# Kernel optimization log

Measured on AMD Instinct MI355X. Metric: run time of the kernel, lower is better.

## Reference

```python
import jax, jax.numpy as jnp
import numpy as np

B, NQ, NKV, D, H, E, FF = 2, 1024, 2048, 1024, 16, 8, 4096
DH = D // H


def _ln(x, g, b):
    m = x.mean(-1, keepdims=True)
    v = ((x - m) ** 2).mean(-1, keepdims=True)
    return (x - m) / jnp.sqrt(v + 1e-5) * g + b


def _mha(q, kv, in_w, in_b, out_w, out_b):
    # torch nn.MultiheadAttention, batch_first=True, dropout=0 (eval)
    wq, wk, wv = jnp.split(in_w, 3, axis=0)   # each [D, D]
    bq, bk, bv = jnp.split(in_b, 3)
    qp = q @ wq.T + bq
    kp = kv @ wk.T + bk
    vp = kv @ wv.T + bv

    def heads(x):
        b, t, _ = x.shape
        return x.reshape(b, t, H, DH).transpose(0, 2, 1, 3)  # [b,H,t,DH]

    qh, kh, vh = heads(qp), heads(kp), heads(vp)
    scores = jnp.einsum('bhqd,bhkd->bhqk', qh, kh) / jnp.sqrt(jnp.float32(DH))
    att = jax.nn.softmax(scores, axis=-1)
    o = jnp.einsum('bhqk,bhkd->bhqd', att, vh)
    o = o.transpose(0, 2, 1, 3).reshape(q.shape[0], q.shape[1], D)
    return o @ out_w.T + out_b


def _moe_token(x, rw, rb, nw, nb, w1, b1, w2, b2, top_k, key):
    # SparseMoE_token: per-token noisy top-k routing.
    logits = x @ rw.T + rb                      # [B,T,E]
    noise_logits = x @ nw.T + nb
    noise = jax.random.normal(key, logits.shape, logits.dtype) * jax.nn.softplus(noise_logits)
    noisy = logits + noise
    _, idx = jax.lax.top_k(noisy, top_k)        # [B,T,K]
    mask = jax.nn.one_hot(idx, E, dtype=noisy.dtype).sum(-2) > 0   # [B,T,E]
    probs = jax.nn.softmax(jnp.where(mask, noisy, -jnp.inf), axis=-1)
    # Dense expert compute weighted by sparse router probs (zeros for
    # non-selected experts) — math identical to masked gather/scatter.
    h = jax.nn.gelu(jnp.einsum('btd,edh->beth', x, w1) + b1[None, :, None, :],
                    approximate=False)          # [B,E,T,FF]
    eo = jnp.einsum('beth,ehd->betd', h, w2) + b2[None, :, None, :]
    return jnp.einsum('bte,betd->btd', probs, eo)


def reference(q, kv,
              ln_cq_g, ln_cq_b, ln_ckv_g, ln_ckv_b, ln_s_g, ln_s_b, ln_m_g, ln_m_b,
              ca_in_w, ca_in_b, ca_out_w, ca_out_b,
              sa_in_w, sa_in_b, sa_out_w, sa_out_b,
              moe_rw, moe_rb, moe_nw, moe_nb, moe_w1, moe_b1, moe_w2, moe_b2,
              top_k):
    key = jax.random.key(42)
    x = _mha(_ln(q, ln_cq_g, ln_cq_b), _ln(kv, ln_ckv_g, ln_ckv_b),
             ca_in_w, ca_in_b, ca_out_w, ca_out_b) + q
    xs = _ln(x, ln_s_g, ln_s_b)
    x = _mha(xs, xs, sa_in_w, sa_in_b, sa_out_w, sa_out_b) + x
    x = _moe_token(_ln(x, ln_m_g, ln_m_b), moe_rw, moe_rb, moe_nw, moe_nb,
                   moe_w1, moe_b1, moe_w2, moe_b2, top_k, key) + x
    return x


def setup_inputs() -> dict:
    key = jax.random.key(0)
    ks = jax.random.split(key, 16)
    s = 0.02
    return {
        'q':  jax.random.normal(ks[0], (B, NQ, D), jnp.float32),
        'kv': jax.random.normal(ks[1], (B, NKV, D), jnp.float32),
        'ln_cq_g': jnp.ones((D,), jnp.float32),  'ln_cq_b': jnp.zeros((D,), jnp.float32),
        'ln_ckv_g': jnp.ones((D,), jnp.float32), 'ln_ckv_b': jnp.zeros((D,), jnp.float32),
        'ln_s_g': jnp.ones((D,), jnp.float32),   'ln_s_b': jnp.zeros((D,), jnp.float32),
        'ln_m_g': jnp.ones((D,), jnp.float32),   'ln_m_b': jnp.zeros((D,), jnp.float32),
        'ca_in_w':  jax.random.normal(ks[2], (3 * D, D), jnp.float32) * s,
        'ca_in_b':  jnp.zeros((3 * D,), jnp.float32),
        'ca_out_w': jax.random.normal(ks[3], (D, D), jnp.float32) * s,
        'ca_out_b': jnp.zeros((D,), jnp.float32),
        'sa_in_w':  jax.random.normal(ks[4], (3 * D, D), jnp.float32) * s,
        'sa_in_b':  jnp.zeros((3 * D,), jnp.float32),
        'sa_out_w': jax.random.normal(ks[5], (D, D), jnp.float32) * s,
        'sa_out_b': jnp.zeros((D,), jnp.float32),
        'moe_rw': jax.random.normal(ks[6], (E, D), jnp.float32) * s,
        'moe_rb': jnp.zeros((E,), jnp.float32),
        'moe_nw': jax.random.normal(ks[7], (E, D), jnp.float32) * s,
        'moe_nb': jnp.zeros((E,), jnp.float32),
        'moe_w1': jax.random.normal(ks[8], (E, D, FF), jnp.float32) * s,
        'moe_b1': jnp.zeros((E, FF), jnp.float32),
        'moe_w2': jax.random.normal(ks[9], (E, FF, D), jnp.float32) * s,
        'moe_b2': jnp.zeros((E, D), jnp.float32),
        'top_k': 2,
    }
```

## Files before the change

### kernel.cpp

```cpp
#include <hip/hip_runtime.h>
#include <cstdint>
#include <cstddef>

#define JAX_THREEFRY_PARTITIONABLE 1

typedef unsigned short u16;
typedef unsigned int u32;
typedef __attribute__((ext_vector_type(8))) short bf16x8;
typedef __attribute__((ext_vector_type(4))) float f32x4;

struct Ptr8 { u16* p[8]; };

struct QkvArgs {
  const u16* ah[3]; const u16* al[3];
  const u16* wh[3]; const u16* wl[3];
  const float* bias[3];
  float* c[3];
  int M[3];
};

__device__ __forceinline__ int imin_(int a, int b) { return a < b ? a : b; }

__device__ __forceinline__ void gl16_(const void* g, void* l) {
  __builtin_amdgcn_global_load_lds(
// ... 67 lines not shown
    p = fmaf(p, w, 0.00134934322f);
    p = fmaf(p, w, -0.00367342844f);
    p = fmaf(p, w, 0.00573950773f);
    p = fmaf(p, w, -0.0076224613f);
    p = fmaf(p, w, 0.00943887047f);
    p = fmaf(p, w, 1.00167406f);
    p = fmaf(p, w, 2.83297682f);
  }
  return p * x;
}

__device__ float bits_to_normal_(unsigned b) {
  const float lo = -0.99999994f;
  float f = __uint_as_float((b >> 9) | 0x3f800000u) - 1.0f;
  float u = fmaxf(lo, f * 2.0f + lo);
  return 1.41421356237f * erfinv_f32_(u);
}

__global__ __launch_bounds__(256) void noise_kernel(float* __restrict__ normals) {
  int i = blockIdx.x * 256 + threadIdx.x;
#if JAX_THREEFRY_PARTITIONABLE
  if (i < 16384) {
    unsigned o0, o1;
    threefry2x32_(0u, 42u, 0u, (unsigned)i, o0, o1);
    normals[i] = bits_to_normal_(o0 ^ o1);
  }
#else
  if (i < 8192) {
    unsigned o0, o1;
    threefry2x32_(0u, 42u, (unsigned)i, (unsigned)(i + 8192), o0, o1);
    normals[i] = bits_to_normal_(o0);
    normals[i + 8192] = bits_to_normal_(o1);
  }
#endif
}

__device__ float block_reduce_sum_(float v) {
  for (int m = 1; m <= 32; m <<= 1) v += __shfl_xor(v, m, 64);
  __shared__ float red[4];
  int lane = threadIdx.x & 63, w = threadIdx.x >> 6;
  if (lane == 0) red[w] = v;
  __syncthreads();
  v = red[0] + red[1] + red[2] + red[3];
  __syncthreads();
  return v;
}

__global__ __launch_bounds__(256) void ln_kernel(
    const float* __restrict__ X, const float* __restrict__ g,
    const float* __restrict__ bta, float* __restrict__ Y) {
  int row = blockIdx.x;
  int t = threadIdx.x;
  const float4* xr = (const float4*)(X + (size_t)row * 1024);
  float4 v = xr[t];
  float s = v.x + v.y + v.z + v.w;
  s = block_reduce_sum_(s);
  float mean = s * (1.0f / 1024.0f);
  float dx = v.x - mean, dy = v.y - mean, dz = v.z - mean, dw = v.w - mean;
  float sq = dx * dx + dy * dy + dz * dz + dw * dw;
  sq = block_reduce_sum_(sq);
  float rstd = 1.0f / sqrtf(sq * (1.0f / 1024.0f) + 1e-5f);
  float4 gv = ((const float4*)g)[t];
  float4 bv = ((const float4*)bta)[t];
  float4 y;
  y.x = dx * rstd * gv.x + bv.x;
  y.y = dy * rstd * gv.y + bv.y;
  y.z = dz * rstd * gv.z + bv.z;
  y.w = dw * rstd * gv.w + bv.w;
  ((float4*)(Y + (size_t)row * 1024))[t] = y;
}

__global__ __launch_bounds__(256) void ln_split_kernel(
    const float* __restrict__ X, const float* __restrict__ g,
    const float* __restrict__ bta, u16* __restrict__ Yh,
    u16* __restrict__ Yl) {
  int row = blockIdx.x;
  int t = threadIdx.x;
  const float4* xr = (const float4*)(X + (size_t)row * 1024);
  float4 v = xr[t];
  float s = v.x + v.y + v.z + v.w;
  s = block_reduce_sum_(s);
  float mean = s * (1.0f / 1024.0f);
  float dx = v.x - mean, dy = v.y - mean, dz = v.z - mean, dw = v.w - mean;
  float sq = dx * dx + dy * dy + dz * dz + dw * dw;
  sq = block_reduce_sum_(sq);
  float rstd = 1.0f / sqrtf(sq * (1.0f / 1024.0f) + 1e-5f);
  float4 gv = ((const float4*)g)[t];
  float4 bv = ((const float4*)bta)[t];
  float y[4];
  y[0] = dx * rstd * gv.x + bv.x;
  y[1] = dy * rstd * gv.y + bv.y;
  y[2] = dz * rstd * gv.z + bv.z;
  y[3] = dw * rstd * gv.w + bv.w;
  ushort4 h, l;
  u16* hp = (u16*)&h; u16* lp = (u16*)&l;
#pragma unroll
  for (int j = 0; j < 4; ++j) {
    u16 hh = f2bf_(y[j]);
    hp[j] = hh;
    lp[j] = f2bf_(y[j] - bf2f_(hh));
  }
  *(ushort4*)(Yh + (size_t)row * 1024 + t * 4) = h;
  *(ushort4*)(Yl + (size_t)row * 1024 + t * 4) = l;
}

__global__ __launch_bounds__(256) void cvt_split_kernel(
    const float* __restrict__ src, u16* __restrict__ hi,
    u16* __restrict__ lo) {
  int i = (blockIdx.x * 256 + threadIdx.x) * 4;
  float4 v = *(const float4*)(src + i);
  float a[4] = {v.x, v.y, v.z, v.w};
  ushort4 h, l;
  u16* hp = (u16*)&h; u16* lp = (u16*)&l;
#pragma unroll
  for (int j = 0; j < 4; ++j) {
    u16 hh = f2bf_(a[j]);
    hp[j] = hh;
    lp[j] = f2bf_(a[j] - bf2f_(hh));
  }
  *(ushort4*)(hi + i) = h;
  *(ushort4*)(lo + i) = l;
}

__global__ __launch_bounds__(256) void tcvt_kernel(
    const float* __restrict__ src, Ptr8 dst, int R, int C) {
  __shared__ float tile[64][65];
  const int e = blockIdx.z;
  const float* S = src + (size_t)e * R * C;
  u16* D = dst.p[e];
  const int c0 = blockIdx.x * 64, r0 = blockIdx.y * 64;
  const int t = threadIdx.x;
  const int tr = t >> 4, tc = (t & 15) * 4;
#pragma unroll
  for (int p = 0; p < 4; ++p) {
    float4 v = *(const float4*)(S + (size_t)(r0 + p * 16 + tr) * C + c0 + tc);
    tile[p * 16 + tr][tc + 0] = v.x;
    tile[p * 16 + tr][tc + 1] = v.y;
    tile[p * 16 + tr][tc + 2] = v.z;
    tile[p * 16 + tr][tc + 3] = v.w;
  }
  __syncthreads();
#pragma unroll
  for (int p = 0; p < 4; ++p) {
    int oc = p * 16 + tr;
    ushort4 o;
    o.x = f2bf_(tile[tc + 0][oc]);
    o.y = f2bf_(tile[tc + 1][oc]);
    o.z = f2bf_(tile[tc + 2][oc]);
    o.w = f2bf_(tile[tc + 3][oc]);
    *(ushort4*)(D + (size_t)(c0 + oc) * R + r0 + tc) = o;
  }
}

template<bool RESID>
__device__ __forceinline__ void split_gemm_body_(
    const u16* __restrict__ Ah, const u16* __restrict__ Al,
    const u16* __restrict__ Wh, const u16* __restrict__ Wl,
    const float* __restrict__ bias, const float* __restrict__ resid,
    float* __restrict__ C, int m0, int n0, int N, int K) {
  __shared__ __align__(16) u16 Ahs[128 * 32];
  __shared__ __align__(16) u16 Als[128 * 32];
  __shared__ __align__(16) u16 Bhs[128 * 32];
  __shared__ __align__(16) u16 Bls[128 * 32];
  const int t = threadIdx.x;
  const int lane = t & 63, wv = t >> 6;
  const int wm = (wv & 1) * 64, wn = (wv >> 1) * 64;
  const int col = lane & 15, quad = lane >> 4;
  f32x4 acc[4][4] = {};
  const int r0 = t >> 2, kq = (t & 3) * 8;
  const u16* pah0 = Ah + (size_t)(m0 + r0) * K + kq;
  const u16* pah1 = Ah + (size_t)(m0 + r0 + 64) * K + kq;
  const u16* pal0 = Al + (size_t)(m0 + r0) * K + kq;
  const u16* pal1 = Al + (size_t)(m0 + r0 + 64) * K + kq;
  const u16* pwh0 = Wh + (size_t)(n0 + r0) * K + kq;
  const u16* pwh1 = Wh + (size_t)(n0 + r0 + 64) * K + kq;
  const u16* pwl0 = Wl + (size_t)(n0 + r0) * K + kq;
  const u16* pwl1 = Wl + (size_t)(n0 + r0 + 64) * K + kq;
  u16* lah0 = &Ahs[t * 8];       u16* lah1 = &Ahs[(t + 256) * 8];
  u16* lal0 = &Als[t * 8];       u16* lal1 = &Als[(t + 256) * 8];
  u16* lbh0 = &Bhs[t * 8];       u16* lbh1 = &Bhs[(t + 256) * 8];
  u16* lbl0 = &Bls[t * 8];       u16* lbl1 = &Bls[(t + 256) * 8];
  for (int k0 = 0; k0 < K; k0 += 32) {
    gl16_(pah0, lah0); gl16_(pah1, lah1);
    gl16_(pal0, lal0); gl16_(pal1, lal1);
    gl16_(pwh0, lbh0); gl16_(pwh1, lbh1);
    gl16_(pwl0, lbl0); gl16_(pwl1, lbl1);
    pah0 += 32; pah1 += 32; pal0 += 32; pal1 += 32;
    pwh0 += 32; pwh1 += 32; pwl0 += 32; pwl1 += 32;
    __syncthreads();
    bf16x8 afh[4], afl[4], bfh[4], bfl[4];
#pragma unroll
    for (int i = 0; i < 4; ++i) {
      afh[i] = *(const bf16x8*)&Ahs[(wm + i * 16 + col) * 32 + quad * 8];
      afl[i] = *(const bf16x8*)&Als[(wm + i * 16 + col) * 32 + quad * 8];
    }
#pragma unroll
    for (int j = 0; j < 4; ++j) {
      bfh[j] = *(const bf16x8*)&Bhs[(wn + j * 16 + col) * 32 + quad * 8];
      bfl[j] = *(const bf16x8*)&Bls[(wn + j * 16 + col) * 32 + quad * 8];
    }
#pragma unroll
    for (int i = 0; i < 4; ++i) {
#pragma unroll
      for (int j = 0; j < 4; ++j) {
        acc[i][j] = __builtin_amdgcn_mfma_f32_16x16x32_bf16(afh[i], bfh[j], acc[i][j], 0, 0, 0);
        acc[i][j] = __builtin_amdgcn_mfma_f32_16x16x32_bf16(afh[i], bfl[j], acc[i][j], 0, 0, 0);
        acc[i][j] = __builtin_amdgcn_mfma_f32_16x16x32_bf16(afl[i], bfh[j], acc[i][j], 0, 0, 0);
      }
    }
    __syncthreads();
  }
  float bv[4];
#pragma unroll
  for (int j = 0; j < 4; ++j) bv[j] = bias[n0 + wn + j * 16 + col];
#pragma unroll
  for (int i = 0; i < 4; ++i) {
#pragma unroll
    for (int rr = 0; rr < 4; ++rr) {
      int m = m0 + wm + i * 16 + quad * 4 + rr;
      float* crow = C + (size_t)m * N;
      const float* rrow = RESID ? (resid + (size_t)m * N) : nullptr;
#pragma unroll
      for (int j = 0; j < 4; ++j) {
        int n = n0 + wn + j * 16 + col;
        float v = acc[i][j][rr] + bv[j];
        if (RESID) v += rrow[n];
        crow[n] = v;
      }
    }
  }
}

template<bool RESID>
__global__ __launch_bounds__(256) void split_gemm_nt(
    const u16* __restrict__ Ah, const u16* __restrict__ Al,
    const u16* __restrict__ Wh, const u16* __restrict__ Wl,
    const float* __restrict__ bias, const float* __restrict__ resid,
    float* __restrict__ C, int M, int N, int K) {
  (void)M;
  split_gemm_body_<RESID>(Ah, Al, Wh, Wl, bias, resid, C,
                          blockIdx.y * 128, blockIdx.x * 128, N, K);
}

__global__ __launch_bounds__(256) void split_gemm_qkv(QkvArgs a, int N, int K) {
  const int z = blockIdx.z;
  const int m0 = blockIdx.y * 128;
  if (m0 >= a.M[z]) return;
  split_gemm_body_<false>(a.ah[z], a.al[z], a.wh[z], a.wl[z], a.bias[z],
                          nullptr, a.c[z], m0, blockIdx.x * 128, N, K);
}

__global__ __launch_bounds__(256) void attn_kernel(
    const float* __restrict__ QP, const float* __restrict__ KP,
    const float* __restrict__ VP, u16* __restrict__ AOh,
    u16* __restrict__ AOl, int nq, int nkv) {
  __shared__ __align__(16) u16 Ksh[64 * 72];
  __shared__ __align__(16) u16 Ksl[64 * 72];
  __shared__ __align__(16) u16 Vth[64 * 72];
  __shared__ __align__(16) u16 Vtl[64 * 72];
  const int t = threadIdx.x;
  const int lane = t & 63, wv = t >> 6;
  const int col = lane & 15, quad = lane >> 4;
  const int bh = blockIdx.x;
  const int b = bh >> 4, h = bh & 15;
  const int q0 = blockIdx.y * 64;
  const int wq0 = wv * 16;

  bf16x8 qbh[2], qbl[2];
  {
    const float* qsrc =
        QP + (size_t)(b * nq + q0 + wq0 + col) * 1024 + h * 64 + quad * 8;
#pragma unroll
    for (int ks = 0; ks < 2; ++ks) {
      float4 f0 = *(const float4*)(qsrc + ks * 32);
      float4 f1 = *(const float4*)(qsrc + ks * 32 + 4);
      float qf[8] = {f0.x, f0.y, f0.z, f0.w, f1.x, f1.y, f1.z, f1.w};
      FragU uh, ul;
#pragma unroll
      for (int w = 0; w < 4; ++w)
        split2_(qf[2 * w] * 0.125f, qf[2 * w + 1] * 0.125f, uh.w[w], ul.w[w]);
      qbh[ks] = uh.v;
      qbl[ks] = ul.v;
    }
  }

  f32x4 o[4] = {};
  float mi = -INFINITY, li = 0.0f;

  const int kr = t >> 2, kc = (t & 3) * 16;
  const int vg = t >> 5, vr = (t & 31) * 2;

  for (int kv0 = 0; kv0 < nkv; kv0 += 64) {
    {
      const float* ksrc =
          KP + (size_t)(b * nkv + kv0 + kr) * 1024 + h * 64 + kc;
      float4 f0 = *(const float4*)(ksrc);
      float4 f1 = *(const float4*)(ksrc + 4);
      float4 f2 = *(const float4*)(ksrc + 8);
      float4 f3 = *(const float4*)(ksrc + 12);
      float kf[16] = {f0.x, f0.y, f0.z, f0.w, f1.x, f1.y, f1.z, f1.w,
                      f2.x, f2.y, f2.z, f2.w, f3.x, f3.y, f3.z, f3.w};
      FragU h0, h1, l0, l1;
#pragma unroll
      for (int w = 0; w < 4; ++w) {
        split2_(kf[2 * w], kf[2 * w + 1], h0.w[w], l0.w[w]);
        split2_(kf[8 + 2 * w], kf[9 + 2 * w], h1.w[w], l1.w[w]);
      }
      *(uint4*)&Ksh[kr * 72 + kc] = h0.q;
      *(uint4*)&Ksh[kr * 72 + kc + 8] = h1.q;
      *(uint4*)&Ksl[kr * 72 + kc] = l0.q;
      *(uint4*)&Ksl[kr * 72 + kc + 8] = l1.q;
    }
    {
      const float* vsrc =
          VP + (size_t)(b * nkv + kv0 + vr) * 1024 + h * 64 + vg * 8;
      float4 a0 = *(const float4*)(vsrc);
      float4 a1 = *(const float4*)(vsrc + 4);
      float4 b0 = *(const float4*)(vsrc + 1024);
      float4 b1 = *(const float4*)(vsrc + 1028);
      float va[8] = {a0.x, a0.y, a0.z, a0.w, a1.x, a1.y, a1.z, a1.w};
      float vb[8] = {b0.x, b0.y, b0.z, b0.w, b1.x, b1.y, b1.z, b1.w};
#pragma unroll
      for (int e = 0; e < 8; ++e) {
        u32 hh, ll;
        split2_(va[e], vb[e], hh, ll);
        *(u32*)&Vth[(vg * 8 + e) * 72 + vr] = hh;
        *(u32*)&Vtl[(vg * 8 + e) * 72 + vr] = ll;
      }
    }
    __syncthreads();

    f32x4 st[4] = {};
#pragma unroll
    for (int ks = 0; ks < 2; ++ks) {
      bf16x8 kah[4], kal[4];
#pragma unroll
      for (int i = 0; i < 4; ++i) {
        kah[i] = *(const bf16x8*)&Ksh[(i * 16 + col) * 72 + ks * 32 + quad * 8];
        kal[i] = *(const bf16x8*)&Ksl[(i * 16 + col) * 72 + ks * 32 + quad * 8];
      }
#pragma unroll
      for (int i = 0; i < 4; ++i) {
        st[i] = __builtin_amdgcn_mfma_f32_16x16x32_bf16(kah[i], qbh[ks], st[i], 0, 0, 0);
        st[i] = __builtin_amdgcn_mfma_f32_16x16x32_bf16(kah[i], qbl[ks], st[i], 0, 0, 0);
        st[i] = __builtin_amdgcn_mfma_f32_16x16x32_bf16(kal[i], qbh[ks], st[i], 0, 0, 0);
      }
    }

    float tmax = st[0][0];
#pragma unroll
    for (int i = 0; i < 4; ++i)
#pragma unroll
      for (int r = 0; r < 4; ++r) tmax = fmaxf(tmax, st[i][r]);
    tmax = fmaxf(tmax, __shfl_xor(tmax, 16, 64));
    tmax = fmaxf(tmax, __shfl_xor(tmax, 32, 64));
    float mnew = fmaxf(mi, tmax);
    float alpha = __expf(mi - mnew);
    float tsum = 0.0f;
#pragma unroll
    for (int i = 0; i < 4; ++i) {
#pragma unroll
      for (int r = 0; r < 4; ++r) {
        float p = __expf(st[i][r] - mnew);
        st[i][r] = p;
        tsum += p;
      }
    }
    tsum += __shfl_xor(tsum, 16, 64);
    tsum += __shfl_xor(tsum, 32, 64);
    li = li * alpha + tsum;
    mi = mnew;
    float alr[4];
#pragma unroll
    for (int r = 0; r < 4; ++r)
      alr[r] = __shfl(alpha, (lane & 48) | (quad * 4 + r), 64);
#pragma unroll
    for (int j = 0; j < 4; ++j)
#pragma unroll
      for (int r = 0; r < 4; ++r) o[j][r] *= alr[r];

    u32 pkh[4][2], pkl[4][2];
#pragma unroll
    for (int i = 0; i < 4; ++i)
#pragma unroll
      for (int w = 0; w < 2; ++w)
        split2_(st[i][2 * w], st[i][2 * w + 1], pkh[i][w], pkl[i][w]);
    u32 APh[2][4], APl[2][4];
    const int par = quad >> 1;
#pragma unroll
    for (int i = 0; i < 4; ++i) {
#pragma unroll
      for (int w01 = 0; w01 < 2; ++w01) {
#pragma unroll
        for (int dw = 0; dw < 2; ++dw) {
          int src = (((2 * quad + dw) & 3) << 4) | col;
          u32 vh = (u32)__shfl((int)pkh[i][w01], src, 64);
          u32 vl = (u32)__shfl((int)pkl[i][w01], src, 64);
          if ((i & 1) == par) {
            APh[i >> 1][dw * 2 + w01] = vh;
            APl[i >> 1][dw * 2 + w01] = vl;
          }
        }
      }
    }

#pragma unroll
    for (int ks = 0; ks < 2; ++ks) {
      FragU fh, fl;
#pragma unroll
      for (int w = 0; w < 4; ++w) { fh.w[w] = APh[ks][w]; fl.w[w] = APl[ks][w]; }
      bf16x8 pah = fh.v, pal = fl.v;
#pragma unroll
      for (int j = 0; j < 4; ++j) {
        bf16x8 vbh = *(const bf16x8*)&Vth[(j * 16 + col) * 72 + ks * 32 + quad * 8];
        bf16x8 vbl = *(const bf16x8*)&Vtl[(j * 16 + col) * 72 + ks * 32 + quad * 8];
        o[j] = __builtin_amdgcn_mfma_f32_16x16x32_bf16(pah, vbh, o[j], 0, 0, 0);
        o[j] = __builtin_amdgcn_mfma_f32_16x16x32_bf16(pah, vbl, o[j], 0, 0, 0);
        o[j] = __builtin_amdgcn_mfma_f32_16x16x32_bf16(pal, vbh, o[j], 0, 0, 0);
      }
    }
    __syncthreads();
  }

  float inv = 1.0f / li;
  float ivr[4];
#pragma unroll
  for (int r = 0; r < 4; ++r)
    ivr[r] = __shfl(inv, (lane & 48) | (quad * 4 + r), 64);
#pragma unroll
  for (int r = 0; r < 4; ++r) {
    size_t base =
        (size_t)(b * nq + q0 + wq0 + quad * 4 + r) * 1024 + h * 64 + col;
#pragma unroll
    for (int j = 0; j < 4; ++j) {
      float v = o[j][r] * ivr[r];
      u16 hh = f2bf_(v);
      AOh[base + j * 16] = hh;
      AOl[base + j * 16] = f2bf_(v - bf2f_(hh));
    }
  }
}

__global__ __launch_bounds__(256) void router_kernel(
    const float* __restrict__ xm, const float* __restrict__ rw,
    const float* __restrict__ rb, const float* __restrict__ nw,
    const float* __restrict__ nb, float* __restrict__ logits,
    float* __restrict__ nlogits) {
  int row = blockIdx.x, t = threadIdx.x;
  const float* x = xm + (size_t)row * 1024;
  float accl[8] = {}, accn[8] = {};
  for (int d = t; d < 1024; d += 256) {
    float xv = x[d];
#pragma unroll
    for (int e = 0; e < 8; ++e) {
      accl[e] += xv * rw[e * 1024 + d];
      accn[e] += xv * nw[e * 1024 + d];
    }
  }
  __shared__ float red[16][4];
  int lane = t & 63, w = t >> 6;
#pragma unroll
  for (int e = 0; e < 8; ++e) {
    float v = accl[e];
    for (int m = 1; m <= 32; m <<= 1) v += __shfl_xor(v, m, 64);
    if (lane == 0) red[e][w] = v;
    float v2 = accn[e];
    for (int m = 1; m <= 32; m <<= 1) v2 += __shfl_xor(v2, m, 64);
    if (lane == 0) red[8 + e][w] = v2;
  }
  __syncthreads();
  if (t < 8)
    logits[row * 8 + t] = red[t][0] + red[t][1] + red[t][2] + red[t][3] + rb[t];
  else if (t < 16)
    nlogits[row * 8 + t - 8] =
        red[t][0] + red[t][1] + red[t][2] + red[t][3] + nb[t - 8];
}

__global__ __launch_bounds__(256) void route_kernel(
    const float* __restrict__ logits, const float* __restrict__ nlogits,
    const float* __restrict__ normals, int* __restrict__ routei,
    float* __restrict__ routep, int* __restrict__ cnt) {
  int bt = blockIdx.x * 256 + threadIdx.x;
  if (bt >= 2048) return;
  float noisy[8];
#pragma unroll
  for (int e = 0; e < 8; ++e) {
    float nl = nlogits[bt * 8 + e];
    float sp = fmaxf(nl, 0.0f) + log1pf(expf(-fabsf(nl)));
    noisy[e] = logits[bt * 8 + e] + normals[bt * 8 + e] * sp;
  }
  int i1 = 0; float n1 = noisy[0];
#pragma unroll
  for (int e = 1; e < 8; ++e) if (noisy[e] > n1) { n1 = noisy[e]; i1 = e; }
  int i2 = -1; float n2 = -INFINITY;
#pragma unroll
  for (int e = 0; e < 8; ++e)
    if (e != i1 && noisy[e] > n2) { n2 = noisy[e]; i2 = e; }
  float e2 = expf(n2 - n1);
  float denom = 1.0f + e2;
  routei[bt * 2 + 0] = i1; routei[bt * 2 + 1] = i2;
  routep[bt * 2 + 0] = 1.0f / denom; routep[bt * 2 + 1] = e2 / denom;
  atomicAdd(&cnt[i1], 1);
  atomicAdd(&cnt[i2], 1);
}

__global__ void zero_kernel(int* __restrict__ cnt) {
  if (threadIdx.x < 8) cnt[threadIdx.x] = 0;
}

__global__ void offs_kernel(const int* __restrict__ cnt, int* __restrict__ offs,
                            int* __restrict__ fill) {
  if (threadIdx.x == 0 && blockIdx.x == 0) {
    int o = 0;
    for (int e = 0; e < 8; ++e) { offs[e] = o; o += cnt[e]; fill[e] = 0; }
  }
}

__global__ __launch_bounds__(256) void fill_kernel(
    const int* __restrict__ routei, const float* __restrict__ routep,
    const int* __restrict__ offs, int* __restrict__ fill,
    int* __restrict__ alist, float* __restrict__ aprob) {
  int bt = blockIdx.x * 256 + threadIdx.x;
  if (bt >= 2048) return;
#pragma unroll
  for (int s = 0; s < 2; ++s) {
    int e = routei[bt * 2 + s];
    int pos = offs[e] + atomicAdd(&fill[e], 1);
    alist[pos] = bt;
    aprob[pos] = routep[bt * 2 + s];
  }
}

__global__ __launch_bounds__(256) void copy_kernel(const float* __restrict__ src,
                                                   float* __restrict__ dst) {
  int i = blockIdx.x * 256 + threadIdx.x;
  ((float4*)dst)[i] = ((const float4*)src)[i];
}

__global__ __launch_bounds__(256) void f2bf_kernel(const float* __restrict__ src,
                                                   u16* __restrict__ dst) {
  int i = (blockIdx.x * 256 + threadIdx.x) * 4;
  float4 v = *(const float4*)(src + i);
  ushort4 o;
  o.x = f2bf_(v.x); o.y = f2bf_(v.y); o.z = f2bf_(v.z); o.w = f2bf_(v.w);
  *(ushort4*)(dst + i) = o;
}

__device__ __forceinline__ float gelu_exact_(float x) {
  return 0.5f * x * (1.0f + erff(x * 0.70710678f));
}

__global__ __launch_bounds__(256) void ffn1_mfma(
    const u16* __restrict__ Xb, Ptr8 w1t, const float* __restrict__ B1,
    u16* __restrict__ H, const int* __restrict__ alist,
    const int* __restrict__ cnt, const int* __restrict__ offs) {
  const int e = blockIdx.z;
  const int ce = cnt[e];
  const int m0 = blockIdx.y * 128;
  if (m0 >= ce) return;
  const int off = offs[e];
  const int n0 = blockIdx.x * 128;
  const u16* __restrict__ WT = w1t.p[e];
  __shared__ __align__(16) u16 As[128 * 32];
  __shared__ __align__(16) u16 Bs[128 * 32];
  const int t = threadIdx.x;
  const int lane = t & 63, wv = t >> 6;
  const int wm = (wv & 1) * 64, wn = (wv >> 1) * 64;
  const int col = lane & 15, quad = lane >> 4;
  f32x4 acc[4][4] = {};
  const int r0 = t >> 2, kq = (t & 3) * 8;
  const int arow0 = alist[off + imin_(m0 + r0, ce - 1)];
  const int arow1 = alist[off + imin_(m0 + r0 + 64, ce - 1)];
  const u16* pa0 = Xb + (size_t)arow0 * 1024 + kq;
  const u16* pa1 = Xb + (size_t)arow1 * 1024 + kq;
  const u16* pw0 = WT + (size_t)(n0 + r0) * 1024 + kq;
  const u16* pw1 = WT + (size_t)(n0 + r0 + 64) * 1024 + kq;
  u16* la0 = &As[t * 8]; u16* la1 = &As[(t + 256) * 8];
  u16* lb0 = &Bs[t * 8]; u16* lb1 = &Bs[(t + 256) * 8];
  for (int k0 = 0; k0 < 1024; k0 += 32) {
    gl16_(pa0, la0); gl16_(pa1, la1);
    gl16_(pw0, lb0); gl16_(pw1, lb1);
    pa0 += 32; pa1 += 32; pw0 += 32; pw1 += 32;
    __syncthreads();
    bf16x8 af[4], bf[4];
#pragma unroll
    for (int i = 0; i < 4; ++i)
      af[i] = *(const bf16x8*)&As[(wm + i * 16 + col) * 32 + quad * 8];
#pragma unroll
    for (int j = 0; j < 4; ++j)
      bf[j] = *(const bf16x8*)&Bs[(wn + j * 16 + col) * 32 + quad * 8];
#pragma unroll
    for (int i = 0; i < 4; ++i)
#pragma unroll
      for (int j = 0; j < 4; ++j)
        acc[i][j] = __builtin_amdgcn_mfma_f32_16x16x32_bf16(af[i], bf[j], acc[i][j], 0, 0, 0);
    __syncthreads();
  }
#pragma unroll
  for (int j = 0; j < 4; ++j) {
    int n = n0 + wn + j * 16 + col;
    float bv = B1[(size_t)e * 4096 + n];
#pragma unroll
    for (int i = 0; i < 4; ++i) {
#pragma unroll
      for (int r2 = 0; r2 < 4; ++r2) {
        int m = m0 + wm + i * 16 + quad * 4 + r2;
        if (m < ce) {
          float v = gelu_exact_(acc[i][j][r2] + bv);
          H[(size_t)(off + m) * 4096 + n] = f2bf_(v);
        }
      }
    }
  }
}

__global__ __launch_bounds__(256) void ffn2_mfma(
    const u16* __restrict__ H, Ptr8 w2t, const float* __restrict__ B2,
    float* __restrict__ Out, const int* __restrict__ alist,
    const float* __restrict__ aprob, const int* __restrict__ cnt,
    const int* __restrict__ offs) {
  const int e = blockIdx.z;
  const int ce = cnt[e];
  const int mt = blockIdx.y >> 2, ks = blockIdx.y & 3;
  const int m0 = mt * 128;
  if (m0 >= ce) return;
  const int off = offs[e];
  const int n0 = blockIdx.x * 128;
  const u16* __restrict__ WT = w2t.p[e];
  __shared__ __align__(16) u16 As[128 * 32];
  __shared__ __align__(16) u16 Bs[128 * 32];
  const int t = threadIdx.x;
  const int lane = t & 63, wv = t >> 6;
  const int wm = (wv & 1) * 64, wn = (wv >> 1) * 64;
  const int col = lane & 15, quad = lane >> 4;
  f32x4 acc[4][4] = {};
  const int r0 = t >> 2, kq = (t & 3) * 8;
  const u16* pa0 =
      H + (size_t)(off + imin_(m0 + r0, ce - 1)) * 4096 + ks * 1024 + kq;
  const u16* pa1 =
      H + (size_t)(off + imin_(m0 + r0 + 64, ce - 1)) * 4096 + ks * 1024 + kq;
  const u16* pw0 = WT + (size_t)(n0 + r0) * 4096 + ks * 1024 + kq;
  const u16* pw1 = WT + (size_t)(n0 + r0 + 64) * 4096 + ks * 1024 + kq;
  u16* la0 = &As[t * 8]; u16* la1 = &As[(t + 256) * 8];
  u16* lb0 = &Bs[t * 8]; u16* lb1 = &Bs[(t + 256) * 8];
  for (int k0 = 0; k0 < 1024; k0 += 32) {
    gl16_(pa0, la0); gl16_(pa1, la1);
    gl16_(pw0, lb0); gl16_(pw1, lb1);
    pa0 += 32; pa1 += 32; pw0 += 32; pw1 += 32;
    __syncthreads();
    bf16x8 af[4], bf[4];
#pragma unroll
    for (int i = 0; i < 4; ++i)
      af[i] = *(const bf16x8*)&As[(wm + i * 16 + col) * 32 + quad * 8];
#pragma unroll
    for (int j = 0; j < 4; ++j)
      bf[j] = *(const bf16x8*)&Bs[(wn + j * 16 + col) * 32 + quad * 8];
#pragma unroll
    for (int i = 0; i < 4; ++i)
#pragma unroll
      for (int j = 0; j < 4; ++j)
        acc[i][j] = __builtin_amdgcn_mfma_f32_16x16x32_bf16(af[i], bf[j], acc[i][j], 0, 0, 0);
    __syncthreads();
  }
  float bv[4];
#pragma unroll
  for (int j = 0; j < 4; ++j)
    bv[j] = (ks == 0) ? B2[(size_t)e * 1024 + n0 + wn + j * 16 + col] : 0.0f;
#pragma unroll
  for (int i = 0; i < 4; ++i) {
#pragma unroll
    for (int r2 = 0; r2 < 4; ++r2) {
      int m = m0 + wm + i * 16 + quad * 4 + r2;
      if (m < ce) {
        int aidx = off + m;
        int tok = alist[aidx];
        float p = aprob[aidx];
        float* orow = Out + (size_t)tok * 1024;
#pragma unroll
        for (int j = 0; j < 4; ++j) {
          int n = n0 + wn + j * 16 + col;
          atomicAdd(&orow[n], p * (acc[i][j][r2] + bv[j]));
        }
      }
    }
  }
}

extern "C" void kernel_launch(void* const* d_in, const int* in_sizes, int n_in,
                              void* d_out, int out_size, void* d_ws, size_t ws_size,
                              hipStream_t stream) {
  (void)in_sizes; (void)n_in; (void)out_size; (void)ws_size;
  const float* q        = (const float*)d_in[0];
  const float* kv       = (const float*)d_in[1];
  const float* ln_cq_g  = (const float*)d_in[2];
  const float* ln_cq_b  = (const float*)d_in[3];
  const float* ln_ckv_g = (const float*)d_in[4];
  const float* ln_ckv_b = (const float*)d_in[5];
  const float* ln_s_g   = (const float*)d_in[6];
  const float* ln_s_b   = (const float*)d_in[7];
  const float* ln_m_g   = (const float*)d_in[8];
  const float* ln_m_b   = (const float*)d_in[9];
  const float* ca_in_w  = (const float*)d_in[10];
  const float* ca_in_b  = (const float*)d_in[11];
  const float* ca_out_w = (const float*)d_in[12];
  const float* ca_out_b = (const float*)d_in[13];
  const float* sa_in_w  = (const float*)d_in[14];
  const float* sa_in_b  = (const float*)d_in[15];
  const float* sa_out_w = (const float*)d_in[16];
  const float* sa_out_b = (const float*)d_in[17];
  const float* moe_rw   = (const float*)d_in[18];
  const float* moe_rb   = (const float*)d_in[19];
  const float* moe_nw   = (const float*)d_in[20];
  const float* moe_nb   = (const float*)d_in[21];
  const float* moe_w1   = (const float*)d_in[22];
  const float* moe_b1   = (const float*)d_in[23];
  const float* moe_w2   = (const float*)d_in[24];
  const float* moe_b2   = (const float*)d_in[25];
  float* out = (float*)d_out;

  float* ws = (float*)d_ws;
  const size_t MEG = 1u << 20;
  float* x1   = ws;
  float* x2   = ws + 2 * MEG;
  float* xm   = ws + 4 * MEG;
  u16*   aoh  = (u16*)(ws + 6 * MEG);
  u16*   aol  = (u16*)(ws + 7 * MEG);
  float* misc = ws + 8 * MEG;
  float* normals = misc;
  float* logits  = misc + 16384;
  float* nlogits = misc + 32768;
  float* routep  = misc + 49152;
  float* aprob   = misc + 53248;
  int*   routei  = (int*)(misc + 57344);
  int*   alist   = (int*)(misc + 61440);
  int*   cnt     = (int*)(misc + 65536);
  int*   offs    = cnt + 8;
  int*   fillc   = cnt + 16;
  float* RA = ws + 8 * MEG + 131072;
  u16*   w1h = (u16*)RA;
  u16*   w1l = (u16*)(RA + (3 * MEG) / 2);
  u16*   w2h = (u16*)(RA + 3 * MEG);
  u16*   w2l = (u16*)(RA + 3 * MEG + MEG / 2);
  u16*   a1h = (u16*)(RA + 4 * MEG);
  u16*   a1l = (u16*)(RA + 5 * MEG);
  u16*   a2h = (u16*)(RA + 6 * MEG);
  u16*   a2l = (u16*)(RA + 8 * MEG);
  float* qp  = RA + 10 * MEG;
  float* kp  = RA + 12 * MEG;
  float* vp  = RA + 16 * MEG;
  u16*   xb  = (u16*)RA;
  u16*   hb  = (u16*)(RA + 1 * MEG);
  Ptr8 wt;
  wt.p[0] = (u16*)(RA + 9 * MEG);
  wt.p[1] = (u16*)(RA + 11 * MEG);
  wt.p[2] = (u16*)(RA + 13 * MEG);
  wt.p[3] = (u16*)(RA + 15 * MEG);
  wt.p[4] = (u16*)(RA + 17 * MEG);
  wt.p[5] = (u16*)x1;
  wt.p[6] = (u16*)xm;
  wt.p[7] = (u16*)(ws + 6 * MEG);

  dim3 blk(256);

  zero_kernel<<<dim3(1), blk, 0, stream>>>(cnt);
  noise_kernel<<<dim3(64), blk, 0, stream>>>(normals);

  cvt_split_kernel<<<dim3(3072), blk, 0, stream>>>(ca_in_w, w1h, w1l);
  cvt_split_kernel<<<dim3(1024), blk, 0, stream>>>(ca_out_w, w2h, w2l);
  ln_split_kernel<<<dim3(2048), blk, 0, stream>>>(q, ln_cq_g, ln_cq_b, a1h, a1l);
  ln_split_kernel<<<dim3(4096), blk, 0, stream>>>(kv, ln_ckv_g, ln_ckv_b, a2h, a2l);
  {
    QkvArgs qa;
    qa.ah[0] = a1h; qa.al[0] = a1l;
    qa.ah[1] = a2h; qa.al[1] = a2l;
    qa.ah[2] = a2h; qa.al[2] = a2l;
    for (int z = 0; z < 3; ++z) {
      qa.wh[z] = w1h + (size_t)z * MEG;
      qa.wl[z] = w1l + (size_t)z * MEG;
      qa.bias[z] = ca_in_b + z * 1024;
    }
    qa.c[0] = qp; qa.c[1] = kp; qa.c[2] = vp;
    qa.M[0] = 2048; qa.M[1] = 4096; qa.M[2] = 4096;
    split_gemm_qkv<<<dim3(8, 32, 3), blk, 0, stream>>>(qa, 1024, 1024);
  }
  attn_kernel<<<dim3(32, 16), blk, 0, stream>>>(qp, kp, vp, aoh, aol, 1024, 2048);
  split_gemm_nt<true><<<dim3(8, 16), blk, 0, stream>>>(
      aoh, aol, w2h, w2l, ca_out_b, q, x1, 2048, 1024, 1024);

  cvt_split_kernel<<<dim3(3072), blk, 0, stream>>>(sa_in_w, w1h, w1l);
  cvt_split_kernel<<<dim3(1024), blk, 0, stream>>>(sa_out_w, w2h, w2l);
  ln_split_kernel<<<dim3(2048), blk, 0, stream>>>(x1, ln_s_g, ln_s_b, a1h, a1l);
  {
    QkvArgs qa;
    for (int z = 0; z < 3; ++z) {
      qa.ah[z] = a1h; qa.al[z] = a1l;
      qa.wh[z] = w1h + (size_t)z * MEG;
      qa.wl[z] = w1l + (size_t)z * MEG;
      qa.bias[z] = sa_in_b + z * 1024;
      qa.M[z] = 2048;
    }
    qa.c[0] = qp; qa.c[1] = kp; qa.c[2] = vp;
    split_gemm_qkv<<<dim3(8, 16, 3), blk, 0, stream>>>(qa, 1024, 1024);
  }
  attn_kernel<<<dim3(32, 16), blk, 0, stream>>>(qp, kp, vp, aoh, aol, 1024, 1024);
  split_gemm_nt<true><<<dim3(8, 16), blk, 0, stream>>>(
      aoh, aol, w2h, w2l, sa_out_b, x1, x2, 2048, 1024, 1024);

  ln_kernel<<<dim3(2048), blk, 0, stream>>>(x2, ln_m_g, ln_m_b, xm);
  f2bf_kernel<<<dim3(2048), blk, 0, stream>>>(xm, xb);
  router_kernel<<<dim3(2048), blk, 0, stream>>>(xm, moe_rw, moe_rb, moe_nw, moe_nb, logits, nlogits);
  route_kernel<<<dim3(8), blk, 0, stream>>>(logits, nlogits, normals, routei, routep, cnt);
  offs_kernel<<<dim3(1), blk, 0, stream>>>(cnt, offs, fillc);
  fill_kernel<<<dim3(8), blk, 0, stream>>>(routei, routep, offs, fillc, alist, aprob);
  copy_kernel<<<dim3(2048), blk, 0, stream>>>(x2, out);
  tcvt_kernel<<<dim3(64, 16, 8), blk, 0, stream>>>(moe_w1, wt, 1024, 4096);
  ffn1_mfma<<<dim3(32, 16, 8), blk, 0, stream>>>(xb, wt, moe_b1, hb, alist, cnt, offs);
  tcvt_kernel<<<dim3(16, 64, 8), blk, 0, stream>>>(moe_w2, wt, 4096, 1024);
  ffn2_mfma<<<dim3(8, 64, 8), blk, 0, stream>>>(hb, wt, moe_b2, out, alist, aprob, cnt, offs);
}
```

Before: 1.069 ms.

## Pre-split K/V into swizzled bf16, prefetch tiles, split-K atomic out-proj

```diff
diff --git a/kernel.cpp b/kernel.cpp
--- a/kernel.cpp
+++ b/kernel.cpp
@@ -243,12 +243,79 @@
   }
 }
 
-template<bool RESID>
+__global__ __launch_bounds__(256) void ksp_k_kernel(
+    const float* __restrict__ KP, u16* __restrict__ Kh,
+    u16* __restrict__ Kl, int nkv) {
+  const int bh = blockIdx.x;
+  const int b = bh >> 4, h = bh & 15;
+  const int kv0 = blockIdx.y * 64;
+  const int t = threadIdx.x;
+  const int kvl = t >> 2, dh0 = (t & 3) * 16;
+  const int kv = kv0 + kvl;
+  const float* src = KP + (size_t)(b * nkv + kv) * 1024 + h * 64 + dh0;
+  float f[16];
+  *(float4*)(f + 0)  = *(const float4*)(src + 0);
+  *(float4*)(f + 4)  = *(const float4*)(src + 4);
+  *(float4*)(f + 8)  = *(const float4*)(src + 8);
+  *(float4*)(f + 12) = *(const float4*)(src + 12);
+  size_t rowb = ((size_t)bh * nkv + kv) * 64;
+#pragma unroll
+  for (int pi = 0; pi < 2; ++pi) {
+    int p = (t & 3) * 2 + pi;
+    FragU hq, lq;
+#pragma unroll
+    for (int w = 0; w < 4; ++w)
+      split2_(f[pi * 8 + 2 * w], f[pi * 8 + 2 * w + 1], hq.w[w], lq.w[w]);
+    int q = p ^ (kvl & 7);
+    *(uint4*)&Kh[rowb + q * 8] = hq.q;
+    *(uint4*)&Kl[rowb + q * 8] = lq.q;
+  }
+}
+
+__global__ __launch_bounds__(256) void ksp_v_kernel(
+    const float* __restrict__ VP, u16* __restrict__ Vh,
+    u16* __restrict__ Vl, int nkv) {
+  __shared__ float tile[64][65];
+  const int bh = blockIdx.x;
+  const int b = bh >> 4, h = bh & 15;
+  const int kv0 = blockIdx.y * 64;
+  const int t = threadIdx.x;
+  {
+    const int kvl = t >> 2, dh0 = (t & 3) * 16;
+    const float* src =
+        VP + (size_t)(b * nkv + kv0 + kvl) * 1024 + h * 64 + dh0;
+#pragma unroll
+    for (int j = 0; j < 4; ++j) {
+      float4 v = *(const float4*)(src + 4 * j);
+      tile[kvl][dh0 + 4 * j + 0] = v.x;
+      tile[kvl][dh0 + 4 * j + 1] = v.y;
+      tile[kvl][dh0 + 4 * j + 2] = v.z;
+      tile[kvl][dh0 + 4 * j + 3] = v.w;
+    }
+  }
+  __syncthreads();
+  const int dh = t >> 2;
+  size_t rowb = ((size_t)bh * 64 + dh) * nkv + kv0;
+#pragma unroll
+  for (int pi = 0; pi < 2; ++pi) {
+    int p = (t & 3) * 2 + pi;
+    FragU hq, lq;
+#pragma unroll
+    for (int w = 0; w < 4; ++w)
+      split2_(tile[p * 8 + 2 * w][dh], tile[p * 8 + 2 * w + 1][dh],
+              hq.w[w], lq.w[w]);
+    int q = p ^ (dh & 7);
+    *(uint4*)&Vh[rowb + q * 8] = hq.q;
+    *(uint4*)&Vl[rowb + q * 8] = lq.q;
+  }
+}
+
+template<bool ATOMIC>
 __device__ __forceinline__ void split_gemm_body_(
     const u16* __restrict__ Ah, const u16* __restrict__ Al,
     const u16* __restrict__ Wh, const u16* __restrict__ Wl,
-    const float* __restrict__ bias, const float* __restrict__ resid,
-    float* __restrict__ C, int m0, int n0, int N, int K) {
+    const float* __restrict__ bias, int addb, float* __restrict__ C,
+    int m0, int n0, int N, int K, int kbeg, int klen) {
   __shared__ __align__(16) u16 Ahs[128 * 32];
   __shared__ __align__(16) u16 Als[128 * 32];
   __shared__ __align__(16) u16 Bhs[128 * 32];
@@ -259,25 +326,27 @@
   const int col = lane & 15, quad = lane >> 4;
   f32x4 acc[4][4] = {};
   const int r0 = t >> 2, kq = (t & 3) * 8;
-  const u16* pah0 = Ah + (size_t)(m0 + r0) * K + kq;
-  const u16* pah1 = Ah + (size_t)(m0 + r0 + 64) * K + kq;
-  const u16* pal0 = Al + (size_t)(m0 + r0) * K + kq;
-  const u16* pal1 = Al + (size_t)(m0 + r0 + 64) * K + kq;
-  const u16* pwh0 = Wh + (size_t)(n0 + r0) * K + kq;
-  const u16* pwh1 = Wh + (size_t)(n0 + r0 + 64) * K + kq;
-  const u16* pwl0 = Wl + (size_t)(n0 + r0) * K + kq;
-  const u16* pwl1 = Wl + (size_t)(n0 + r0 + 64) * K + kq;
-  u16* lah0 = &Ahs[t * 8];       u16* lah1 = &Ahs[(t + 256) * 8];
-  u16* lal0 = &Als[t * 8];       u16* lal1 = &Als[(t + 256) * 8];
-  u16* lbh0 = &Bhs[t * 8];       u16* lbh1 = &Bhs[(t + 256) * 8];
-  u16* lbl0 = &Bls[t * 8];       u16* lbl1 = &Bls[(t + 256) * 8];
-  for (int k0 = 0; k0 < K; k0 += 32) {
-    gl16_(pah0, lah0); gl16_(pah1, lah1);
-    gl16_(pal0, lal0); gl16_(pal1, lal1);
-    gl16_(pwh0, lbh0); gl16_(pwh1, lbh1);
-    gl16_(pwl0, lbl0); gl16_(pwl1, lbl1);
-    pah0 += 32; pah1 += 32; pal0 += 32; pal1 += 32;
-    pwh0 += 32; pwh1 += 32; pwl0 += 32; pwl1 += 32;
+  const u16* pah0 = Ah + (size_t)(m0 + r0) * K + kbeg + kq;
+  const u16* pah1 = Ah + (size_t)(m0 + r0 + 64) * K + kbeg + kq;
+  const u16* pal0 = Al + (size_t)(m0 + r0) * K + kbeg + kq;
+  const u16* pal1 = Al + (size_t)(m0 + r0 + 64) * K + kbeg + kq;
+  const u16* pwh0 = Wh + (size_t)(n0 + r0) * K + kbeg + kq;
+  const u16* pwh1 = Wh + (size_t)(n0 + r0 + 64) * K + kbeg + kq;
+  const u16* pwl0 = Wl + (size_t)(n0 + r0) * K + kbeg + kq;
+  const u16* pwl1 = Wl + (size_t)(n0 + r0 + 64) * K + kbeg + kq;
+  u16* lah0 = &Ahs[t * 8]; u16* lah1 = &Ahs[(t + 256) * 8];
+  u16* lal0 = &Als[t * 8]; u16* lal1 = &Als[(t + 256) * 8];
+  u16* lbh0 = &Bhs[t * 8]; u16* lbh1 = &Bhs[(t + 256) * 8];
+  u16* lbl0 = &Bls[t * 8]; u16* lbl1 = &Bls[(t + 256) * 8];
+#define SG_ISSUE() do { \
+    gl16_(pah0, lah0); gl16_(pah1, lah1); \
+    gl16_(pal0, lal0); gl16_(pal1, lal1); \
+    gl16_(pwh0, lbh0); gl16_(pwh1, lbh1); \
+    gl16_(pwl0, lbl0); gl16_(pwl1, lbl1); \
+    pah0 += 32; pah1 += 32; pal0 += 32; pal1 += 32; \
+    pwh0 += 32; pwh1 += 32; pwl0 += 32; pwl1 += 32; } while (0)
+  SG_ISSUE();
+  for (int k0 = 0; k0 < klen; k0 += 32) {
     __syncthreads();
     bf16x8 afh[4], afl[4], bfh[4], bfl[4];
 #pragma unroll
@@ -290,6 +359,8 @@
       bfh[j] = *(const bf16x8*)&Bhs[(wn + j * 16 + col) * 32 + quad * 8];
       bfl[j] = *(const bf16x8*)&Bls[(wn + j * 16 + col) * 32 + quad * 8];
     }
+    __syncthreads();
+    if (k0 + 32 < klen) SG_ISSUE();
 #pragma unroll
     for (int i = 0; i < 4; ++i) {
 #pragma unroll
@@ -299,56 +370,56 @@
         acc[i][j] = __builtin_amdgcn_mfma_f32_16x16x32_bf16(afl[i], bfh[j], acc[i][j], 0, 0, 0);
       }
     }
-    __syncthreads();
-  }
+  }
+#undef SG_ISSUE
   float bv[4];
 #pragma unroll
-  for (int j = 0; j < 4; ++j) bv[j] = bias[n0 + wn + j * 16 + col];
+  for (int j = 0; j < 4; ++j)
+    bv[j] = (!ATOMIC || addb) ? bias[n0 + wn + j * 16 + col] : 0.0f;
 #pragma unroll
   for (int i = 0; i < 4; ++i) {
 #pragma unroll
     for (int rr = 0; rr < 4; ++rr) {
       int m = m0 + wm + i * 16 + quad * 4 + rr;
       float* crow = C + (size_t)m * N;
-      const float* rrow = RESID ? (resid + (size_t)m * N) : nullptr;
 #pragma unroll
       for (int j = 0; j < 4; ++j) {
         int n = n0 + wn + j * 16 + col;
         float v = acc[i][j][rr] + bv[j];
-        if (RESID) v += rrow[n];
-        crow[n] = v;
+        if (ATOMIC) atomicAdd(&crow[n], v);
+        else crow[n] = v;
       }
     }
   }
-}
-
-template<bool RESID>
-__global__ __launch_bounds__(256) void split_gemm_nt(
-    const u16* __restrict__ Ah, const u16* __restrict__ Al,
-    const u16* __restrict__ Wh, const u16* __restrict__ Wl,
-    const float* __restrict__ bias, const float* __restrict__ resid,
-    float* __restrict__ C, int M, int N, int K) {
-  (void)M;
-  split_gemm_body_<RESID>(Ah, Al, Wh, Wl, bias, resid, C,
-                          blockIdx.y * 128, blockIdx.x * 128, N, K);
 }
 
 __global__ __launch_bounds__(256) void split_gemm_qkv(QkvArgs a, int N, int K) {
   const int z = blockIdx.z;
   const int m0 = blockIdx.y * 128;
   if (m0 >= a.M[z]) return;
-  split_gemm_body_<false>(a.ah[z], a.al[z], a.wh[z], a.wl[z], a.bias[z],
-                          nullptr, a.c[z], m0, blockIdx.x * 128, N, K);
+  split_gemm_body_<false>(a.ah[z], a.al[z], a.wh[z], a.wl[z], a.bias[z], 1,
+                          a.c[z], m0, blockIdx.x * 128, N, K, 0, K);
+}
+
+__global__ __launch_bounds__(256) void split_gemm_atomic(
+    const u16* __restrict__ Ah, const u16* __restrict__ Al,
+    const u16* __restrict__ Wh, const u16* __restrict__ Wl,
+    const float* __restrict__ bias, float* __restrict__ C, int N, int K) {
+  const int ks = blockIdx.z;
+  split_gemm_body_<true>(Ah, Al, Wh, Wl, bias, ks == 0 ? 1 : 0, C,
+                         blockIdx.y * 128, blockIdx.x * 128, N, K,
+                         ks * (K >> 1), K >> 1);
 }
 
 __global__ __launch_bounds__(256) void attn_kernel(
-    const float* __restrict__ QP, const float* __restrict__ KP,
-    const float* __restrict__ VP, u16* __restrict__ AOh,
+    const float* __restrict__ QP, const u16* __restrict__ Khg,
+    const u16* __restrict__ Klg, const u16* __restrict__ Vhg,
+    const u16* __restrict__ Vlg, u16* __restrict__ AOh,
     u16* __restrict__ AOl, int nq, int nkv) {
-  __shared__ __align__(16) u16 Ksh[64 * 72];
-  __shared__ __align__(16) u16 Ksl[64 * 72];
-  __shared__ __align__(16) u16 Vth[64 * 72];
-  __shared__ __align__(16) u16 Vtl[64 * 72];
+  __shared__ __align__(16) u16 Ksh[64 * 64];
+  __shared__ __align__(16) u16 Ksl[64 * 64];
+  __shared__ __align__(16) u16 Vth[64 * 64];
+  __shared__ __align__(16) u16 Vtl[64 * 64];
   const int t = threadIdx.x;
   const int lane = t & 63, wv = t >> 6;
   const int col = lane & 15, quad = lane >> 4;
@@ -356,6 +427,26 @@
   const int b = bh >> 4, h = bh & 15;
   const int q0 = blockIdx.y * 64;
   const int wq0 = wv * 16;
+  const int s1 = t + 256;
+  const size_t krow = (size_t)bh * nkv;
+  const size_t vbase = (size_t)bh * 64 * nkv;
+  const size_t voff0 = (size_t)(t >> 3) * nkv + (t & 7) * 8;
+  const size_t voff1 = (size_t)(s1 >> 3) * nkv + (s1 & 7) * 8;
+
+  {
+    const u16* kb = Khg + krow * 64;
+    const u16* lb = Klg + krow * 64;
+    gl16_(kb + t * 8, &Ksh[t * 8]);
+    gl16_(kb + s1 * 8, &Ksh[s1 * 8]);
+    gl16_(lb + t * 8, &Ksl[t * 8]);
+    gl16_(lb + s1 * 8, &Ksl[s1 * 8]);
+    const u16* vb = Vhg + vbase;
+    const u16* wb = Vlg + vbase;
+    gl16_(vb + voff0, &Vth[t * 8]);
+    gl16_(vb + voff1, &Vth[s1 * 8]);
+    gl16_(wb + voff0, &Vtl[t * 8]);
+    gl16_(wb + voff1, &Vtl[s1 * 8]);
+  }
 
   bf16x8 qbh[2], qbl[2];
   {
@@ -378,47 +469,7 @@
   f32x4 o[4] = {};
   float mi = -INFINITY, li = 0.0f;
 
-  const int kr = t >> 2, kc = (t & 3) * 16;
-  const int vg = t >> 5, vr = (t & 31) * 2;
-
   for (int kv0 = 0; kv0 < nkv; kv0 += 64) {
-    {
-      const float* ksrc =
-          KP + (size_t)(b * nkv + kv0 + kr) * 1024 + h * 64 + kc;
-      float4 f0 = *(const float4*)(ksrc);
-      float4 f1 = *(const float4*)(ksrc + 4);
-      float4 f2 = *(const float4*)(ksrc + 8);
-      float4 f3 = *(const float4*)(ksrc + 12);
-      float kf[16] = {f0.x, f0.y, f0.z, f0.w, f1.x, f1.y, f1.z, f1.w,
-                      f2.x, f2.y, f2.z, f2.w, f3.x, f3.y, f3.z, f3.w};
-      FragU h0, h1, l0, l1;
-#pragma unroll
-      for (int w = 0; w < 4; ++w) {
-        split2_(kf[2 * w], kf[2 * w + 1], h0.w[w], l0.w[w]);
-        split2_(kf[8 + 2 * w], kf[9 + 2 * w], h1.w[w], l1.w[w]);
-      }
-      *(uint4*)&Ksh[kr * 72 + kc] = h0.q;
-      *(uint4*)&Ksh[kr * 72 + kc + 8] = h1.q;
-      *(uint4*)&Ksl[kr * 72 + kc] = l0.q;
-      *(uint4*)&Ksl[kr * 72 + kc + 8] = l1.q;
-    }
-    {
-      const float* vsrc =
-          VP + (size_t)(b * nkv + kv0 + vr) * 1024 + h * 64 + vg * 8;
-      float4 a0 = *(const float4*)(vsrc);
-      float4 a1 = *(const float4*)(vsrc + 4);
-      float4 b0 = *(const float4*)(vsrc + 1024);
-      float4 b1 = *(const float4*)(vsrc + 1028);
-      float va[8] = {a0.x, a0.y, a0.z, a0.w, a1.x, a1.y, a1.z, a1.w};
-      float vb[8] = {b0.x, b0.y, b0.z, b0.w, b1.x, b1.y, b1.z, b1.w};
-#pragma unroll
-      for (int e = 0; e < 8; ++e) {
-        u32 hh, ll;
-        split2_(va[e], vb[e], hh, ll);
-        *(u32*)&Vth[(vg * 8 + e) * 72 + vr] = hh;
-        *(u32*)&Vtl[(vg * 8 + e) * 72 + vr] = ll;
-      }
-    }
     __syncthreads();
 
     f32x4 st[4] = {};
@@ -427,8 +478,9 @@
       bf16x8 kah[4], kal[4];
 #pragma unroll
       for (int i = 0; i < 4; ++i) {
-        kah[i] = *(const bf16x8*)&Ksh[(i * 16 + col) * 72 + ks * 32 + quad * 8];
-        kal[i] = *(const bf16x8*)&Ksl[(i * 16 + col) * 72 + ks * 32 + quad * 8];
+        int addr = (i * 16 + col) * 64 + (((ks << 2) + quad) ^ (col & 7)) * 8;
+        kah[i] = *(const bf16x8*)&Ksh[addr];
+        kal[i] = *(const bf16x8*)&Ksl[addr];
       }
 #pragma unroll
       for (int i = 0; i < 4; ++i) {
@@ -436,6 +488,31 @@
         st[i] = __builtin_amdgcn_mfma_f32_16x16x32_bf16(kah[i], qbl[ks], st[i], 0, 0, 0);
         st[i] = __builtin_amdgcn_mfma_f32_16x16x32_bf16(kal[i], qbh[ks], st[i], 0, 0, 0);
       }
+    }
+    bf16x8 vfh[2][4], vfl[2][4];
+#pragma unroll
+    for (int ks = 0; ks < 2; ++ks) {
+#pragma unroll
+      for (int j = 0; j < 4; ++j) {
+        int addr = (j * 16 + col) * 64 + (((ks << 2) + quad) ^ (col & 7)) * 8;
+        vfh[ks][j] = *(const bf16x8*)&Vth[addr];
+        vfl[ks][j] = *(const bf16x8*)&Vtl[addr];
+      }
+    }
+    __syncthreads();
+    if (kv0 + 64 < nkv) {
+      const u16* kb = Khg + (krow + kv0 + 64) * 64;
+      const u16* lb = Klg + (krow + kv0 + 64) * 64;
+      gl16_(kb + t * 8, &Ksh[t * 8]);
+      gl16_(kb + s1 * 8, &Ksh[s1 * 8]);
+      gl16_(lb + t * 8, &Ksl[t * 8]);
+      gl16_(lb + s1 * 8, &Ksl[s1 * 8]);
+      const u16* vb = Vhg + vbase + kv0 + 64;
+      const u16* wb = Vlg + vbase + kv0 + 64;
+      gl16_(vb + voff0, &Vth[t * 8]);
+      gl16_(vb + voff1, &Vth[s1 * 8]);
+      gl16_(wb + voff0, &Vtl[t * 8]);
+      gl16_(wb + voff1, &Vtl[s1 * 8]);
     }
 
     float tmax = st[0][0];
@@ -503,14 +580,11 @@
       bf16x8 pah = fh.v, pal = fl.v;
 #pragma unroll
       for (int j = 0; j < 4; ++j) {
-        bf16x8 vbh = *(const bf16x8*)&Vth[(j * 16 + col) * 72 + ks * 32 + quad * 8];
-        bf16x8 vbl = *(const bf16x8*)&Vtl[(j * 16 + col) * 72 + ks * 32 + quad * 8];
-        o[j] = __builtin_amdgcn_mfma_f32_16x16x32_bf16(pah, vbh, o[j], 0, 0, 0);
-        o[j] = __builtin_amdgcn_mfma_f32_16x16x32_bf16(pah, vbl, o[j], 0, 0, 0);
-        o[j] = __builtin_amdgcn_mfma_f32_16x16x32_bf16(pal, vbh, o[j], 0, 0, 0);
+        o[j] = __builtin_amdgcn_mfma_f32_16x16x32_bf16(pah, vfh[ks][j], o[j], 0, 0, 0);
+        o[j] = __builtin_amdgcn_mfma_f32_16x16x32_bf16(pah, vfl[ks][j], o[j], 0, 0, 0);
+        o[j] = __builtin_amdgcn_mfma_f32_16x16x32_bf16(pal, vfh[ks][j], o[j], 0, 0, 0);
       }
     }
-    __syncthreads();
   }
 
   float inv = 1.0f / li;
@@ -668,10 +742,11 @@
   const u16* pw1 = WT + (size_t)(n0 + r0 + 64) * 1024 + kq;
   u16* la0 = &As[t * 8]; u16* la1 = &As[(t + 256) * 8];
   u16* lb0 = &Bs[t * 8]; u16* lb1 = &Bs[(t + 256) * 8];
+#define F1_ISSUE() do { \
+    gl16_(pa0, la0); gl16_(pa1, la1); gl16_(pw0, lb0); gl16_(pw1, lb1); \
+    pa0 += 32; pa1 += 32; pw0 += 32; pw1 += 32; } while (0)
+  F1_ISSUE();
   for (int k0 = 0; k0 < 1024; k0 += 32) {
-    gl16_(pa0, la0); gl16_(pa1, la1);
-    gl16_(pw0, lb0); gl16_(pw1, lb1);
-    pa0 += 32; pa1 += 32; pw0 += 32; pw1 += 32;
     __syncthreads();
     bf16x8 af[4], bf[4];
 #pragma unroll
@@ -680,13 +755,15 @@
 #pragma unroll
     for (int j = 0; j < 4; ++j)
       bf[j] = *(const bf16x8*)&Bs[(wn + j * 16 + col) * 32 + quad * 8];
+    __syncthreads();
+    if (k0 + 32 < 1024) F1_ISSUE();
 #pragma unroll
     for (int i = 0; i < 4; ++i)
 #pragma unroll
       for (int j = 0; j < 4; ++j)
         acc[i][j] = __builtin_amdgcn_mfma_f32_16x16x32_bf16(af[i], bf[j], acc[i][j], 0, 0, 0);
-    __syncthreads();
-  }
+  }
+#undef F1_ISSUE
 #pragma unroll
   for (int j = 0; j < 4; ++j) {
     int n = n0 + wn + j * 16 + col;
@@ -734,10 +811,11 @@
   const u16* pw1 = WT + (size_t)(n0 + r0 + 64) * 4096 + ks * 1024 + kq;
   u16* la0 = &As[t * 8]; u16* la1 = &As[(t + 256) * 8];
   u16* lb0 = &Bs[t * 8]; u16* lb1 = &Bs[(t + 256) * 8];
+#define F2_ISSUE() do { \
+    gl16_(pa0, la0); gl16_(pa1, la1); gl16_(pw0, lb0); gl16_(pw1, lb1); \
+    pa0 += 32; pa1 += 32; pw0 += 32; pw1 += 32; } while (0)
+  F2_ISSUE();
   for (int k0 = 0; k0 < 1024; k0 += 32) {
-    gl16_(pa0, la0); gl16_(pa1, la1);
-    gl16_(pw0, lb0); gl16_(pw1, lb1);
-    pa0 += 32; pa1 += 32; pw0 += 32; pw1 += 32;
     __syncthreads();
     bf16x8 af[4], bf[4];
 #pragma unroll
@@ -746,13 +824,15 @@
 #pragma unroll
     for (int j = 0; j < 4; ++j)
       bf[j] = *(const bf16x8*)&Bs[(wn + j * 16 + col) * 32 + quad * 8];
+    __syncthreads();
+    if (k0 + 32 < 1024) F2_ISSUE();
 #pragma unroll
     for (int i = 0; i < 4; ++i)
 #pragma unroll
       for (int j = 0; j < 4; ++j)
         acc[i][j] = __builtin_amdgcn_mfma_f32_16x16x32_bf16(af[i], bf[j], acc[i][j], 0, 0, 0);
-    __syncthreads();
-  }
+  }
+#undef F2_ISSUE
   float bv[4];
 #pragma unroll
   for (int j = 0; j < 4; ++j)
@@ -839,6 +919,10 @@
   float* qp  = RA + 10 * MEG;
   float* kp  = RA + 12 * MEG;
   float* vp  = RA + 16 * MEG;
+  u16*   ksph = (u16*)RA;
+  u16*   kspl = (u16*)(RA + 4 * MEG);
+  u16*   vsph = (u16*)(RA + 6 * MEG);
+  u16*   vspl = (u16*)(RA + 8 * MEG);
   u16*   xb  = (u16*)RA;
   u16*   hb  = (u16*)(RA + 1 * MEG);
   Ptr8 wt;
@@ -874,9 +958,13 @@
     qa.M[0] = 2048; qa.M[1] = 4096; qa.M[2] = 4096;
     split_gemm_qkv<<<dim3(8, 32, 3), blk, 0, stream>>>(qa, 1024, 1024);
   }
-  attn_kernel<<<dim3(32, 16), blk, 0, stream>>>(qp, kp, vp, aoh, aol, 1024, 2048);
-  split_gemm_nt<true><<<dim3(8, 16), blk, 0, stream>>>(
-      aoh, aol, w2h, w2l, ca_out_b, q, x1, 2048, 1024, 1024);
+  ksp_k_kernel<<<dim3(32, 32), blk, 0, stream>>>(kp, ksph, kspl, 2048);
+  ksp_v_kernel<<<dim3(32, 32), blk, 0, stream>>>(vp, vsph, vspl, 2048);
+  attn_kernel<<<dim3(32, 16), blk, 0, stream>>>(qp, ksph, kspl, vsph, vspl,
+                                                aoh, aol, 1024, 2048);
+  copy_kernel<<<dim3(2048), blk, 0, stream>>>(q, x1);
+  split_gemm_atomic<<<dim3(8, 16, 2), blk, 0, stream>>>(
+      aoh, aol, w2h, w2l, ca_out_b, x1, 1024, 1024);
 
   cvt_split_kernel<<<dim3(3072), blk, 0, stream>>>(sa_in_w, w1h, w1l);
   cvt_split_kernel<<<dim3(1024), blk, 0, stream>>>(sa_out_w, w2h, w2l);
@@ -893,9 +981,13 @@
     qa.c[0] = qp; qa.c[1] = kp; qa.c[2] = vp;
     split_gemm_qkv<<<dim3(8, 16, 3), blk, 0, stream>>>(qa, 1024, 1024);
   }
-  attn_kernel<<<dim3(32, 16), blk, 0, stream>>>(qp, kp, vp, aoh, aol, 1024, 1024);
-  split_gemm_nt<true><<<dim3(8, 16), blk, 0, stream>>>(
-      aoh, aol, w2h, w2l, sa_out_b, x1, x2, 2048, 1024, 1024);
+  ksp_k_kernel<<<dim3(32, 16), blk, 0, stream>>>(kp, ksph, kspl, 1024);
+  ksp_v_kernel<<<dim3(32, 16), blk, 0, stream>>>(vp, vsph, vspl, 1024);
+  attn_kernel<<<dim3(32, 16), blk, 0, stream>>>(qp, ksph, kspl, vsph, vspl,
+                                                aoh, aol, 1024, 1024);
+  copy_kernel<<<dim3(2048), blk, 0, stream>>>(x1, x2);
+  split_gemm_atomic<<<dim3(8, 16, 2), blk, 0, stream>>>(
+      aoh, aol, w2h, w2l, sa_out_b, x2, 1024, 1024);
 
   ln_kernel<<<dim3(2048), blk, 0, stream>>>(x2, ln_m_g, ln_m_b, xm);
   f2bf_kernel<<<dim3(2048), blk, 0, stream>>>(xm, xb);
```

Result: faster. 980.2 us (-8.3%).
